# Performance work log

Measured on AMD Instinct MI355X. Metric: run time of the kernel, lower is better.

Reference implementation:

```python
import jax, jax.numpy as jnp
import numpy as np

EPS = 1e-5
D_MODEL, D_INNER, D_STATE, DT_RANK, K = 2048, 4096, 16, 128, 4

def setup_inputs() -> dict:
    key = jax.random.key(0)
    ks = jax.random.split(key, 13)
    B = 128
    s = lambda k, shape, sc=0.02: jax.random.normal(k, shape, jnp.float32) * sc
    return {
        "hidden_states": jax.random.normal(ks[0], (B, 1, D_MODEL), jnp.float32),
        "conv_state": jax.random.normal(ks[1], (B, D_INNER, K - 1), jnp.float32),
        "ssm_state": jax.random.normal(ks[2], (B, D_INNER, D_STATE), jnp.float32),
        "norm_w": jnp.ones((D_MODEL,), jnp.float32),
        "in_proj_w": s(ks[3], (2 * D_INNER, D_MODEL)),           # no bias (HF Mamba default)
        "conv_w": s(ks[4], (D_INNER, K), 0.1),                    # depthwise conv kernel
        "conv_b": s(ks[5], (D_INNER,), 0.1),
        "x_proj_w": s(ks[6], (DT_RANK + 2 * D_STATE, D_INNER)),
        "dt_proj_w": s(ks[7], (D_INNER, DT_RANK)),
        "dt_proj_b": s(ks[8], (D_INNER,), 0.1),
        "A_log": jnp.log(jnp.broadcast_to(jnp.arange(1, D_STATE + 1, dtype=jnp.float32), (D_INNER, D_STATE))),
        "D": jnp.ones((D_INNER,), jnp.float32),
        "out_proj_w": s(ks[9], (D_MODEL, D_INNER)),               # no bias
    }

def reference(hidden_states, conv_state, ssm_state, norm_w, in_proj_w, conv_w, conv_b,
              x_proj_w, dt_proj_w, dt_proj_b, A_log, D, out_proj_w):
    x = hidden_states[:, 0, :]                                   # (B, d_model)
    # RMSNorm (pre-norm)
    normed = x * jax.lax.rsqrt(jnp.mean(x * x, axis=-1, keepdims=True) + EPS) * norm_w
    # in_proj -> gate z and conv branch xc
    xz = normed @ in_proj_w.T                                    # (B, 2*d_inner)
    xc, z = jnp.split(xz, 2, axis=-1)
    # depthwise causal conv, single-step with rolling cache
    conv_in = jnp.concatenate([conv_state, xc[:, :, None]], axis=-1)  # (B, d_inner, K)
    new_conv_state = conv_in[:, :, 1:]
    xact = jax.nn.silu(jnp.sum(conv_in * conv_w[None], axis=-1) + conv_b)  # (B, d_inner)
    # input-dependent SSM params
    proj = xact @ x_proj_w.T                                     # (B, dt_rank + 2*d_state)
    dt_raw = proj[:, :DT_RANK]
    Bmat = proj[:, DT_RANK:DT_RANK + D_STATE]                    # (B, d_state)
    Cmat = proj[:, DT_RANK + D_STATE:]                           # (B, d_state)
    dt = jax.nn.softplus(dt_raw @ dt_proj_w.T + dt_proj_b)       # (B, d_inner)
    A = -jnp.exp(A_log)                                          # (d_inner, d_state)
    dA = jnp.exp(dt[:, :, None] * A[None])                       # (B, d_inner, d_state)
    dB = dt[:, :, None] * Bmat[:, None, :]
    new_ssm_state = ssm_state * dA + dB * xact[:, :, None]
    y = jnp.sum(new_ssm_state * Cmat[:, None, :], axis=-1) + D * xact
    y = y * jax.nn.silu(z)
    out = y @ out_proj_w.T                                       # (B, d_model)
    output = out[:, None, :] + hidden_states                     # residual add
    return output, new_conv_state, new_ssm_state
```

## Files before the change

### kernel.cpp

```cpp
#include <hip/hip_runtime.h>

typedef __attribute__((ext_vector_type(8))) short bf16x8;
typedef __attribute__((ext_vector_type(4))) float f32x4;
typedef __attribute__((ext_vector_type(8))) unsigned short u16x8;
typedef __attribute__((ext_vector_type(2))) unsigned u32x2;

#define DM 2048
#define DI 4096
#define BATCH 128

__device__ __forceinline__ unsigned short f2bf(float f) {
  union { float f; unsigned u; } v; v.f = f;
  unsigned r = v.u + 0x7FFFu + ((v.u >> 16) & 1u);
  return (unsigned short)(r >> 16);
}
__device__ __forceinline__ float bf2f(unsigned short u) {
  union { unsigned u; float f; } v; v.u = (unsigned)u << 16; return v.f;
}
__device__ __forceinline__ unsigned pk2bf(float lo, float hi) {
  unsigned r;
  asm("v_cvt_pk_bf16_f32 %0, %1, %2" : "=v"(r) : "v"(lo), "v"(hi));
  return r;
}
__device__ __forceinline__ float sigm(float x) { return 1.f / (1.f + __expf(-x)); }

constexpr int BK = 64;
constexpr int LDT = BK + 8;

#define LDREGS(AR, ARF, BR, kb_) do {                                                     \
    int kb = (kb_);                                                                       \
    if constexpr (ABF) {                                                                  \
      _Pragma("unroll") for (int i = 0; i < BM / 32; ++i) {                               \
        int idx = tid + i * 256, r = idx >> 3, c = (idx & 7) * 8;                         \
        AR[i] = *(const u16x8*)&((const unsigned short*)Ag)[(long)(m0 + r) * lda + kb + c]; \
      }                                                                                   \
    } else {                                                                              \
      _Pragma("unroll") for (int i = 0; i < BM / 16; ++i) {                               \
        int idx = tid + i * 256, r = idx >> 4, c = (idx & 15) * 4;                        \
        ARF[i] = *(const f32x4*)&((const float*)Ag)[(long)(m0 + r) * lda + kb + c];       \
      }                                                                                   \
    }                                                                                     \
    _Pragma("unroll") for (int i = 0; i < BN / 16; ++i) {                                 \
      int idx = tid + i * 256, r = idx >> 4, c = (idx & 15) * 4;                          \
      BR[i] = *(const f32x4*)&Bg[(long)(n0 + r) * ldb + kb + c];                          \
    }                                                                                     \
  } while (0)

#define STLDS(AR, ARF, BR, buf_) do {                                                     \
    unsigned short* As_ = lds + (buf_) * BUF;                                             \
    unsigned short* Bs_ = As_ + BM * LDT;                                                 \
    if constexpr (ABF) {                                                                  \
      _Pragma("unroll") for (int i = 0; i < BM / 32; ++i) {                               \
        int idx = tid + i * 256, r = idx >> 3, c = (idx & 7) * 8;                         \
        *(u16x8*)&As_[r * LDT + c] = AR[i];                                               \
      }                                                                                   \
    } else {                                                                              \
      _Pragma("unroll") for (int i = 0; i < BM / 16; ++i) {                               \
        int idx = tid + i * 256, r = idx >> 4, c = (idx & 15) * 4;                        \
        u32x2 o; o[0] = pk2bf(ARF[i][0], ARF[i][1]); o[1] = pk2bf(ARF[i][2], ARF[i][3]); \
        *(u32x2*)&As_[r * LDT + c] = o;                                                   \
      }                                                                                   \
    }                                                                                     \
    _Pragma("unroll") for (int i = 0; i < BN / 16; ++i) {                                 \
      int idx = tid + i * 256, r = idx >> 4, c = (idx & 15) * 4;                          \
      u32x2 o; o[0] = pk2bf(BR[i][0], BR[i][1]); o[1] = pk2bf(BR[i][2], BR[i][3]);       \
      *(u32x2*)&Bs_[r * LDT + c] = o;                                                     \
    }                                                                                     \
  } while (0)

#define COMPUTE(buf_) do {                                                                \
    const unsigned short* As_ = lds + (buf_) * BUF;                                       \
    const unsigned short* Bs_ = As_ + BM * LDT;                                           \
    _Pragma("unroll") for (int kk = 0; kk < BK; kk += 32) {                               \
      int kr = kk + lhi * 8;                                                              \
      bf16x8 af[MI], bfr[NF];                                                             \
      _Pragma("unroll") for (int mi = 0; mi < MI; ++mi)                                   \
        af[mi] = *(const bf16x8*)&As_[(wm * (BM / 2) + mi * 16 + llo) * LDT + kr];        \
      _Pragma("unroll") for (int ni = 0; ni < NF; ++ni)                                   \
        bfr[ni] = *(const bf16x8*)&Bs_[(wn * 16 * NF + ni * 16 + llo) * LDT + kr];        \
      _Pragma("unroll") for (int mi = 0; mi < MI; ++mi)                                   \
        _Pragma("unroll") for (int ni = 0; ni < NF; ++ni)                                 \
          acc[mi * NF + ni] = __builtin_amdgcn_mfma_f32_16x16x32_bf16(                    \
              af[mi], bfr[ni], acc[mi * NF + ni], 0, 0, 0);                               \
    }                                                                                     \
  } while (0)

template<int BM, int BN, bool ABF>
__device__ __forceinline__ void gemmMN(const void* Ag, int lda, const float* Bg, int ldb,
                                       int m0, int n0, int k0, int k1, unsigned short* lds,
                                       f32x4* acc) {
  constexpr int NF = BN / 32;
  constexpr int MI = BM / 32;
  constexpr int BUF = (BM + BN) * LDT;
  const int tid = threadIdx.x, lane = tid & 63, wave = tid >> 6;
  const int wm = wave >> 1, wn = wave & 1, llo = lane & 15, lhi = lane >> 4;

  u16x8 ar0[ABF ? BM / 32 : 1], ar1[ABF ? BM / 32 : 1];
  f32x4 arf0[ABF ? 1 : BM / 16], arf1[ABF ? 1 : BM / 16];
  f32x4 br0[BN / 16], br1[BN / 16];

  const int nt = (k1 - k0) / BK;
  LDREGS(ar0, arf0, br0, k0);
  LDREGS(ar1, arf1, br1, k0 + BK);
  STLDS(ar0, arf0, br0, 0);
  __syncthreads();
  int t = 0;
  while (true) {
    if (t + 2 < nt) LDREGS(ar0, arf0, br0, k0 + (t + 2) * BK);
    COMPUTE(0);
    if (t + 1 < nt) STLDS(ar1, arf1, br1, 1);
    __syncthreads();
    if (++t == nt) break;
    if (t + 2 < nt) LDREGS(ar1, arf1, br1, k0 + (t + 2) * BK);
    COMPUTE(1);
    if (t + 1 < nt) STLDS(ar0, arf0, br0, 0);
    __syncthreads();
    if (++t == nt) break;
  }
}

__global__ __launch_bounds__(256) void k1_rmsnorm(const float* __restrict__ hs,
                                                  const float* __restrict__ nw,
                                                  unsigned short* __restrict__ normed) {
  int b = blockIdx.x, tid = threadIdx.x;
  const float* xr = hs + (long)b * DM;
  f32x4 v0 = *(const f32x4*)&xr[tid * 4];
  f32x4 v1 = *(const f32x4*)&xr[(tid + 256) * 4];
  float ss = v0[0]*v0[0] + v0[1]*v0[1] + v0[2]*v0[2] + v0[3]*v0[3]
           + v1[0]*v1[0] + v1[1]*v1[1] + v1[2]*v1[2] + v1[3]*v1[3];
  for (int off = 32; off; off >>= 1) ss += __shfl_xor(ss, off);
  __shared__ float red[4];
  if ((tid & 63) == 0) red[tid >> 6] = ss;
  __syncthreads();
  ss = red[0] + red[1] + red[2] + red[3];
  float rstd = rsqrtf(ss * (1.f / DM) + 1e-5f);
  f32x4 w0 = *(const f32x4*)&nw[tid * 4];
  f32x4 w1 = *(const f32x4*)&nw[(tid + 256) * 4];
  u32x2 o0, o1;
  o0[0] = pk2bf(v0[0] * rstd * w0[0], v0[1] * rstd * w0[1]);
  o0[1] = pk2bf(v0[2] * rstd * w0[2], v0[3] * rstd * w0[3]);
  o1[0] = pk2bf(v1[0] * rstd * w1[0], v1[1] * rstd * w1[1]);
  o1[1] = pk2bf(v1[2] * rstd * w1[2], v1[3] * rstd * w1[3]);
  *(u32x2*)&normed[(long)b * DM + tid * 4] = o0;
  *(u32x2*)&normed[(long)b * DM + (tid + 256) * 4] = o1;
}

__global__ __launch_bounds__(256) void k2_inproj(const unsigned short* __restrict__ normed,
                                                 const float* __restrict__ W,
                                                 float* __restrict__ xzp) {
  __shared__ unsigned short lds[2 * (128 + 64) * LDT];
  f32x4 acc[8] = {};
  int bn = blockIdx.x, sk = blockIdx.y;
  gemmMN<128, 64, true>(normed, DM, W, DM, 0, bn * 64, sk * 512, sk * 512 + 512, lds, acc);
  int tid = threadIdx.x, lane = tid & 63, wave = tid >> 6, wm = wave >> 1, wn = wave & 1;
  int llo = lane & 15, lhi = lane >> 4;
  float* dst = xzp + (long)sk * (BATCH * 8192);
#pragma unroll
  for (int mi = 0; mi < 4; ++mi)
#pragma unroll
    for (int ni = 0; ni < 2; ++ni)
#pragma unroll
      for (int r = 0; r < 4; ++r) {
        int b = wm * 64 + mi * 16 + lhi * 4 + r;
        int n = bn * 64 + wn * 32 + ni * 16 + llo;
        dst[(long)b * 8192 + n] = acc[mi * 2 + ni][r];
      }
}

__global__ __launch_bounds__(256) void e2_conv(const float* __restrict__ xzp,
                                               const float* __restrict__ conv_state,
                                               const float* __restrict__ conv_w,
                                               const float* __restrict__ conv_b,
                                               float* __restrict__ out_ncs,
                                               float* __restrict__ xact_f,
                                               unsigned short* __restrict__ xact_b,
                                               unsigned short* __restrict__ szb) {
  int p = blockIdx.x * 256 + threadIdx.x;
  int b = p >> 12, n = p & 4095;
  long base = (long)b * 8192 + n;
  float xc = 0.f, z = 0.f;
#pragma unroll
  for (int s = 0; s < 4; ++s) {
    xc += xzp[(long)s * (BATCH * 8192) + base];
    z  += xzp[(long)s * (BATCH * 8192) + base + DI];
  }
  const float* cs = conv_state + (long)p * 3;
  float c0 = cs[0], c1 = cs[1], c2 = cs[2];
  f32x4 cw = *(const f32x4*)&conv_w[n * 4];
  float xs = c0 * cw[0] + c1 * cw[1] + c2 * cw[2] + xc * cw[3] + conv_b[n];
  float xa = xs * sigm(xs);
  float* ncs = out_ncs + (long)p * 3;
  ncs[0] = c1; ncs[1] = c2; ncs[2] = xc;
  xact_f[p] = xa;
  xact_b[p] = f2bf(xa);
  szb[p] = f2bf(z * sigm(z));
}

__global__ __launch_bounds__(256) void k3_xproj(const unsigned short* __restrict__ xact_b,
                                                const float* __restrict__ XW,
                                                float* __restrict__ projp) {
  __shared__ unsigned short lds[2 * (128 + 32) * LDT];
  f32x4 acc[4] = {};
  int bn = blockIdx.x, kc = blockIdx.y;
  gemmMN<128, 32, true>(xact_b, DI, XW, DI, 0, bn * 32, kc * 128, kc * 128 + 128, lds, acc);
  int tid = threadIdx.x, lane = tid & 63, wave = tid >> 6, wm = wave >> 1, wn = wave & 1;
  int llo = lane & 15, lhi = lane >> 4;
  int n = bn * 32 + wn * 16 + llo;
  float* dst = projp + (long)kc * (BATCH * 160);
#pragma unroll
  for (int mi = 0; mi < 4; ++mi)
#pragma unroll
    for (int r = 0; r < 4; ++r) {
      int b = wm * 64 + mi * 16 + lhi * 4 + r;
      dst[b * 160 + n] = acc[mi][r];
    }
}

__global__ __launch_bounds__(256) void k3r_reduce(const float* __restrict__ projp,
                                                  float* __restrict__ proj) {
  int t = blockIdx.x * 256 + threadIdx.x;
  f32x4 s = {};
#pragma unroll
  for (int k = 0; k < 32; ++k) {
    f32x4 v = *(const f32x4*)&projp[(long)k * (BATCH * 160) + t * 4];
    s[0] += v[0]; s[1] += v[1]; s[2] += v[2]; s[3] += v[3];
  }
  *(f32x4*)&proj[t * 4] = s;
}

__global__ __launch_bounds__(256) void k45_dtssm(const float* __restrict__ proj,
                                                 const float* __restrict__ DW,
                                                 const float* __restrict__ dtb,
                                                 const float* __restrict__ A_log,
                                                 const float* __restrict__ Dp,
                                                 const float* __restrict__ ssm,
                                                 const float* __restrict__ xact_f,
                                                 const unsigned short* __restrict__ szb,
                                                 float* __restrict__ out_nss,
                                                 unsigned short* __restrict__ yz_b) {
  __shared__ unsigned short lds[2 * (32 + 32) * LDT];
  f32x4 acc[1] = {};
  int nb = blockIdx.x, mb = blockIdx.y;
  gemmMN<32, 32, false>(proj, 160, DW, 128, mb * 32, nb * 32, 0, 128, lds, acc);
  int tid = threadIdx.x, lane = tid & 63, wave = tid >> 6, wm = wave >> 1, wn = wave & 1;
  int llo = lane & 15, lhi = lane >> 4;
  int n = nb * 32 + wn * 16 + llo;
  float dtbn = dtb[n], Dn = Dp[n];
  f32x4 Al0 = *(const f32x4*)&A_log[n * 16];
  f32x4 Al1 = *(const f32x4*)&A_log[n * 16 + 4];
  f32x4 Al2 = *(const f32x4*)&A_log[n * 16 + 8];
  f32x4 Al3 = *(const f32x4*)&A_log[n * 16 + 12];
  float aS[16];
#pragma unroll
  for (int j = 0; j < 4; ++j) {
    aS[j] = -__expf(Al0[j]); aS[4 + j] = -__expf(Al1[j]);
    aS[8 + j] = -__expf(Al2[j]); aS[12 + j] = -__expf(Al3[j]);
  }
#pragma unroll
  for (int r = 0; r < 4; ++r) {
    int b = mb * 32 + wm * 16 + lhi * 4 + r;
    long p = (long)b * DI + n;
    float v = acc[0][r] + dtbn;
    float dtv = (v > 20.f) ? v : log1pf(__expf(v));
    float xa = xact_f[p];
    const float* Bp = proj + b * 160 + 128;
    const float* Cp = proj + b * 160 + 144;
    const float* sp = ssm + p * 16;
    float* np = out_nss + p * 16;
    float y = 0.f;
#pragma unroll
    for (int q = 0; q < 4; ++q) {
      f32x4 sv = *(const f32x4*)&sp[q * 4];
      f32x4 Bv = *(const f32x4*)&Bp[q * 4];
      f32x4 Cv = *(const f32x4*)&Cp[q * 4];
      f32x4 nv;
#pragma unroll
      for (int j = 0; j < 4; ++j) {
        float dA = __expf(dtv * aS[q * 4 + j]);
        nv[j] = sv[j] * dA + dtv * Bv[j] * xa;
        y += nv[j] * Cv[j];
      }
      *(f32x4*)&np[q * 4] = nv;
    }
    yz_b[p] = f2bf((y + Dn * xa) * bf2f(szb[p]));
  }
}

__global__ __launch_bounds__(256) void k5_outproj(const unsigned short* __restrict__ yz_b,
                                                  const float* __restrict__ OW,
                                                  float* __restrict__ op) {
  __shared__ unsigned short lds[2 * (128 + 32) * LDT];
  f32x4 acc[4] = {};
  int bn = blockIdx.x, sk = blockIdx.y;
  gemmMN<128, 32, true>(yz_b, DI, OW, DI, 0, bn * 32, sk * 512, sk * 512 + 512, lds, acc);
  int tid = threadIdx.x, lane = tid & 63, wave = tid >> 6, wm = wave >> 1, wn = wave & 1;
  int llo = lane & 15, lhi = lane >> 4;
  int n = bn * 32 + wn * 16 + llo;
  float* dst = op + (long)sk * (BATCH * DM);
#pragma unroll
  for (int mi = 0; mi < 4; ++mi)
#pragma unroll
    for (int r = 0; r < 4; ++r) {
      int b = wm * 64 + mi * 16 + lhi * 4 + r;
      dst[(long)b * DM + n] = acc[mi][r];
    }
}

__global__ __launch_bounds__(256) void k7_out(const float* __restrict__ op,
                                              const float* __restrict__ hs,
                                              float* __restrict__ outp) {
  int t = blockIdx.x * 256 + threadIdx.x;
  f32x4 s = *(const f32x4*)&hs[t * 4];
#pragma unroll
  for (int k = 0; k < 8; ++k) {
    f32x4 v = *(const f32x4*)&op[(long)k * (BATCH * DM) + t * 4];
    s[0] += v[0]; s[1] += v[1]; s[2] += v[2]; s[3] += v[3];
  }
  *(f32x4*)&outp[t * 4] = s;
}

extern "C" void kernel_launch(void* const* d_in, const int* in_sizes, int n_in, void* d_out,
                              int out_size, void* d_ws, size_t ws_size, hipStream_t stream) {
  const float* hs         = (const float*)d_in[0];
  const float* conv_state = (const float*)d_in[1];
  const float* ssm        = (const float*)d_in[2];
  const float* norm_w     = (const float*)d_in[3];
  const float* in_proj_w  = (const float*)d_in[4];
  const float* conv_w     = (const float*)d_in[5];
  const float* conv_b     = (const float*)d_in[6];
  const float* x_proj_w   = (const float*)d_in[7];
  const float* dt_proj_w  = (const float*)d_in[8];
  const float* dt_proj_b  = (const float*)d_in[9];
  const float* A_log      = (const float*)d_in[10];
  const float* Dp         = (const float*)d_in[11];
  const float* out_proj_w = (const float*)d_in[12];

  float* outp    = (float*)d_out;
  float* out_ncs = outp + 262144;
  float* out_nss = outp + 262144 + 1572864;

  char* ws = (char*)d_ws;
  unsigned short* normed = (unsigned short*)(ws);
  float*          xact_f = (float*)(ws + (1l << 20));
  unsigned short* xact_b = (unsigned short*)(ws + (3l << 20));
  unsigned short* szb    = (unsigned short*)(ws + (4l << 20));
  float*          proj   = (float*)(ws + (5l << 20));
  float*          projp  = (float*)(ws + (6l << 20));
  float*          xzp    = (float*)(ws + (9l << 20));
  float*          op     = (float*)(ws + (25l << 20));
  unsigned short* yz_b   = (unsigned short*)(ws + (34l << 20));

  hipLaunchKernelGGL(k1_rmsnorm, dim3(128), dim3(256), 0, stream, hs, norm_w, normed);
  hipLaunchKernelGGL(k2_inproj, dim3(128, 4), dim3(256), 0, stream, normed, in_proj_w, xzp);
  hipLaunchKernelGGL(e2_conv, dim3(2048), dim3(256), 0, stream, xzp, conv_state, conv_w, conv_b,
                     out_ncs, xact_f, xact_b, szb);
  hipLaunchKernelGGL(k3_xproj, dim3(5, 32), dim3(256), 0, stream, xact_b, x_proj_w, projp);
  hipLaunchKernelGGL(k3r_reduce, dim3(20), dim3(256), 0, stream, projp, proj);
  hipLaunchKernelGGL(k45_dtssm, dim3(128, 4), dim3(256), 0, stream, proj, dt_proj_w, dt_proj_b,
                     A_log, Dp, ssm, xact_f, szb, out_nss, yz_b);
  hipLaunchKernelGGL(k5_outproj, dim3(64, 8), dim3(256), 0, stream, yz_b, out_proj_w, op);
  hipLaunchKernelGGL(k7_out, dim3(256), dim3(256), 0, stream, op, hs, outp);
}
```

Baseline: 77.65 us.

## Load fp32 weights straight into MFMA registers and store in_proj partials as bf16

Adds a skinny GEMM path (gemmS) where each lane loads its fp32 weight fragment from global memory directly into registers and converts it to bf16 for the MFMA. Only the activation tile goes through LDS, which removes the weight LDS staging and halves shared memory per block. In_proj now uses 32-column tiles over twice as many blocks, writes its split-K partials as bf16 instead of fp32, and the GEMM kernels gain a min-blocks occupancy hint. The risk is less coalesced weight loads and some lost precision in the split-K partial sums.

```diff
diff --git a/kernel.cpp b/kernel.cpp
--- a/kernel.cpp
+++ b/kernel.cpp
@@ -4,6 +4,7 @@
 typedef __attribute__((ext_vector_type(4))) float f32x4;
 typedef __attribute__((ext_vector_type(8))) unsigned short u16x8;
 typedef __attribute__((ext_vector_type(2))) unsigned u32x2;
+typedef __attribute__((ext_vector_type(4))) unsigned u32x4u;
 
 #define DM 2048
 #define DI 4096
@@ -27,93 +28,131 @@
 constexpr int BK = 64;
 constexpr int LDT = BK + 8;
 
-#define LDREGS(AR, ARF, BR, kb_) do {                                                     \
-    int kb = (kb_);                                                                       \
-    if constexpr (ABF) {                                                                  \
-      _Pragma("unroll") for (int i = 0; i < BM / 32; ++i) {                               \
-        int idx = tid + i * 256, r = idx >> 3, c = (idx & 7) * 8;                         \
-        AR[i] = *(const u16x8*)&((const unsigned short*)Ag)[(long)(m0 + r) * lda + kb + c]; \
-      }                                                                                   \
-    } else {                                                                              \
-      _Pragma("unroll") for (int i = 0; i < BM / 16; ++i) {                               \
-        int idx = tid + i * 256, r = idx >> 4, c = (idx & 15) * 4;                        \
-        ARF[i] = *(const f32x4*)&((const float*)Ag)[(long)(m0 + r) * lda + kb + c];       \
-      }                                                                                   \
+#define LDA_S(AR, kb_) do { int kb = (kb_);                                   \
+    _Pragma("unroll") for (int i = 0; i < 4; ++i) {                           \
+      int idx = tid + i * 256, r = idx >> 3, c = (idx & 7) * 8;               \
+      AR[i] = *(const u16x8*)&Ab[(long)r * lda + kb + c];                     \
+    } } while (0)
+
+#define STA_S(AR, buf_) do {                                                  \
+    unsigned short* As_ = lds + (buf_) * (128 * LDT);                         \
+    _Pragma("unroll") for (int i = 0; i < 4; ++i) {                           \
+      int idx = tid + i * 256, r = idx >> 3, c = (idx & 7) * 8;               \
+      *(u16x8*)&As_[r * LDT + c] = AR[i];                                     \
+    } } while (0)
+
+#define LDB_S(BB, kb_) do { int kb = (kb_);                                   \
+    const float* bp = &Bg[(long)nrow * ldb + kb + lhi * 8];                   \
+    BB[0] = *(const f32x4*)bp;       BB[1] = *(const f32x4*)(bp + 4);         \
+    BB[2] = *(const f32x4*)(bp + 32); BB[3] = *(const f32x4*)(bp + 36);       \
+  } while (0)
+
+#define CMP_S(buf_, BB) do {                                                  \
+    const unsigned short* As_ = lds + (buf_) * (128 * LDT);                   \
+    _Pragma("unroll") for (int q = 0; q < 2; ++q) {                           \
+      int kr = q * 32 + lhi * 8;                                              \
+      bf16x8 af[4];                                                           \
+      _Pragma("unroll") for (int mi = 0; mi < 4; ++mi)                        \
+        af[mi] = *(const bf16x8*)&As_[(wm * 64 + mi * 16 + llo) * LDT + kr];  \
+      union { u32x4u u; bf16x8 h; } cv;                                       \
+      cv.u[0] = pk2bf(BB[2 * q][0], BB[2 * q][1]);                            \
+      cv.u[1] = pk2bf(BB[2 * q][2], BB[2 * q][3]);                            \
+      cv.u[2] = pk2bf(BB[2 * q + 1][0], BB[2 * q + 1][1]);                    \
+      cv.u[3] = pk2bf(BB[2 * q + 1][2], BB[2 * q + 1][3]);                    \
+      _Pragma("unroll") for (int mi = 0; mi < 4; ++mi)                        \
+        acc[mi] = __builtin_amdgcn_mfma_f32_16x16x32_bf16(af[mi], cv.h, acc[mi], 0, 0, 0); \
+    } } while (0)
+
+__device__ __forceinline__ void gemmS(const unsigned short* __restrict__ Ab, int lda,
+                                      const float* __restrict__ Bg, int ldb,
+                                      int n0, int k0, int k1, unsigned short* lds,
+                                      f32x4* acc) {
+  const int tid = threadIdx.x, lane = tid & 63, wave = tid >> 6;
+  const int wm = wave >> 1, wn = wave & 1, llo = lane & 15, lhi = lane >> 4;
+  const int nrow = n0 + wn * 16 + llo;
+
+  u16x8 ar0[4], ar1[4];
+  f32x4 bB0[4], bB1[4];
+
+  const int nt = (k1 - k0) / BK;
+  LDA_S(ar0, k0);
+  LDA_S(ar1, k0 + BK);
+  LDB_S(bB0, k0);
+  STA_S(ar0, 0);
+  __syncthreads();
+  int t = 0;
+  while (true) {
+    if (t + 1 < nt) LDB_S(bB1, k0 + (t + 1) * BK);
+    if (t + 2 < nt) LDA_S(ar0, k0 + (t + 2) * BK);
+    CMP_S(0, bB0);
+    if (t + 1 < nt) STA_S(ar1, 1);
+    __syncthreads();
+    if (++t == nt) break;
+    if (t + 1 < nt) LDB_S(bB0, k0 + (t + 1) * BK);
+    if (t + 2 < nt) LDA_S(ar1, k0 + (t + 2) * BK);
+    CMP_S(1, bB1);
+    if (t + 1 < nt) STA_S(ar0, 0);
+    __syncthreads();
+    if (++t == nt) break;
+  }
+}
+
+#define LDREGS(ARF, BR, kb_) do { int kb = (kb_);                                         \
+    _Pragma("unroll") for (int i = 0; i < 2; ++i) {                                       \
+      int idx = tid + i * 256, r = idx >> 4, c = (idx & 15) * 4;                          \
+      ARF[i] = *(const f32x4*)&((const float*)Ag)[(long)(m0 + r) * lda + kb + c];         \
     }                                                                                     \
-    _Pragma("unroll") for (int i = 0; i < BN / 16; ++i) {                                 \
+    _Pragma("unroll") for (int i = 0; i < 2; ++i) {                                       \
       int idx = tid + i * 256, r = idx >> 4, c = (idx & 15) * 4;                          \
       BR[i] = *(const f32x4*)&Bg[(long)(n0 + r) * ldb + kb + c];                          \
+    } } while (0)
+
+#define STLDS(ARF, BR, buf_) do {                                                         \
+    unsigned short* As_ = lds + (buf_) * BUF;                                             \
+    unsigned short* Bs_ = As_ + 32 * LDT;                                                 \
+    _Pragma("unroll") for (int i = 0; i < 2; ++i) {                                       \
+      int idx = tid + i * 256, r = idx >> 4, c = (idx & 15) * 4;                          \
+      u32x2 o; o[0] = pk2bf(ARF[i][0], ARF[i][1]); o[1] = pk2bf(ARF[i][2], ARF[i][3]);   \
+      *(u32x2*)&As_[r * LDT + c] = o;                                                     \
     }                                                                                     \
-  } while (0)
-
-#define STLDS(AR, ARF, BR, buf_) do {                                                     \
-    unsigned short* As_ = lds + (buf_) * BUF;                                             \
-    unsigned short* Bs_ = As_ + BM * LDT;                                                 \
-    if constexpr (ABF) {                                                                  \
-      _Pragma("unroll") for (int i = 0; i < BM / 32; ++i) {                               \
-        int idx = tid + i * 256, r = idx >> 3, c = (idx & 7) * 8;                         \
-        *(u16x8*)&As_[r * LDT + c] = AR[i];                                               \
-      }                                                                                   \
-    } else {                                                                              \
-      _Pragma("unroll") for (int i = 0; i < BM / 16; ++i) {                               \
-        int idx = tid + i * 256, r = idx >> 4, c = (idx & 15) * 4;                        \
-        u32x2 o; o[0] = pk2bf(ARF[i][0], ARF[i][1]); o[1] = pk2bf(ARF[i][2], ARF[i][3]); \
-        *(u32x2*)&As_[r * LDT + c] = o;                                                   \
-      }                                                                                   \
-    }                                                                                     \
-    _Pragma("unroll") for (int i = 0; i < BN / 16; ++i) {                                 \
+    _Pragma("unroll") for (int i = 0; i < 2; ++i) {                                       \
       int idx = tid + i * 256, r = idx >> 4, c = (idx & 15) * 4;                          \
       u32x2 o; o[0] = pk2bf(BR[i][0], BR[i][1]); o[1] = pk2bf(BR[i][2], BR[i][3]);       \
       *(u32x2*)&Bs_[r * LDT + c] = o;                                                     \
-    }                                                                                     \
-  } while (0)
+    } } while (0)
 
 #define COMPUTE(buf_) do {                                                                \
     const unsigned short* As_ = lds + (buf_) * BUF;                                       \
-    const unsigned short* Bs_ = As_ + BM * LDT;                                           \
+    const unsigned short* Bs_ = As_ + 32 * LDT;                                           \
     _Pragma("unroll") for (int kk = 0; kk < BK; kk += 32) {                               \
       int kr = kk + lhi * 8;                                                              \
-      bf16x8 af[MI], bfr[NF];                                                             \
-      _Pragma("unroll") for (int mi = 0; mi < MI; ++mi)                                   \
-        af[mi] = *(const bf16x8*)&As_[(wm * (BM / 2) + mi * 16 + llo) * LDT + kr];        \
-      _Pragma("unroll") for (int ni = 0; ni < NF; ++ni)                                   \
-        bfr[ni] = *(const bf16x8*)&Bs_[(wn * 16 * NF + ni * 16 + llo) * LDT + kr];        \
-      _Pragma("unroll") for (int mi = 0; mi < MI; ++mi)                                   \
-        _Pragma("unroll") for (int ni = 0; ni < NF; ++ni)                                 \
-          acc[mi * NF + ni] = __builtin_amdgcn_mfma_f32_16x16x32_bf16(                    \
-              af[mi], bfr[ni], acc[mi * NF + ni], 0, 0, 0);                               \
-    }                                                                                     \
-  } while (0)
-
-template<int BM, int BN, bool ABF>
-__device__ __forceinline__ void gemmMN(const void* Ag, int lda, const float* Bg, int ldb,
+      bf16x8 af = *(const bf16x8*)&As_[(wm * 16 + llo) * LDT + kr];                       \
+      bf16x8 bfr = *(const bf16x8*)&Bs_[(wn * 16 + llo) * LDT + kr];                      \
+      acc[0] = __builtin_amdgcn_mfma_f32_16x16x32_bf16(af, bfr, acc[0], 0, 0, 0);         \
+    } } while (0)
+
+__device__ __forceinline__ void gemm32(const void* Ag, int lda, const float* Bg, int ldb,
                                        int m0, int n0, int k0, int k1, unsigned short* lds,
                                        f32x4* acc) {
-  constexpr int NF = BN / 32;
-  constexpr int MI = BM / 32;
-  constexpr int BUF = (BM + BN) * LDT;
+  constexpr int BUF = 64 * LDT;
   const int tid = threadIdx.x, lane = tid & 63, wave = tid >> 6;
   const int wm = wave >> 1, wn = wave & 1, llo = lane & 15, lhi = lane >> 4;
-
-  u16x8 ar0[ABF ? BM / 32 : 1], ar1[ABF ? BM / 32 : 1];
-  f32x4 arf0[ABF ? 1 : BM / 16], arf1[ABF ? 1 : BM / 16];
-  f32x4 br0[BN / 16], br1[BN / 16];
-
+  f32x4 arf0[2], arf1[2], br0[2], br1[2];
   const int nt = (k1 - k0) / BK;
-  LDREGS(ar0, arf0, br0, k0);
-  LDREGS(ar1, arf1, br1, k0 + BK);
-  STLDS(ar0, arf0, br0, 0);
+  LDREGS(arf0, br0, k0);
+  LDREGS(arf1, br1, k0 + BK);
+  STLDS(arf0, br0, 0);
   __syncthreads();
   int t = 0;
   while (true) {
-    if (t + 2 < nt) LDREGS(ar0, arf0, br0, k0 + (t + 2) * BK);
+    if (t + 2 < nt) LDREGS(arf0, br0, k0 + (t + 2) * BK);
     COMPUTE(0);
-    if (t + 1 < nt) STLDS(ar1, arf1, br1, 1);
+    if (t + 1 < nt) STLDS(arf1, br1, 1);
     __syncthreads();
     if (++t == nt) break;
-    if (t + 2 < nt) LDREGS(ar1, arf1, br1, k0 + (t + 2) * BK);
+    if (t + 2 < nt) LDREGS(arf1, br1, k0 + (t + 2) * BK);
     COMPUTE(1);
-    if (t + 1 < nt) STLDS(ar0, arf0, br0, 0);
+    if (t + 1 < nt) STLDS(arf0, br0, 0);
     __syncthreads();
     if (++t == nt) break;
   }
@@ -145,29 +184,27 @@
   *(u32x2*)&normed[(long)b * DM + (tid + 256) * 4] = o1;
 }
 
-__global__ __launch_bounds__(256) void k2_inproj(const unsigned short* __restrict__ normed,
-                                                 const float* __restrict__ W,
-                                                 float* __restrict__ xzp) {
-  __shared__ unsigned short lds[2 * (128 + 64) * LDT];
-  f32x4 acc[8] = {};
+__global__ __launch_bounds__(256, 4) void k2_inproj(const unsigned short* __restrict__ normed,
+                                                    const float* __restrict__ W,
+                                                    unsigned short* __restrict__ xzp) {
+  __shared__ unsigned short lds[2 * 128 * LDT];
+  f32x4 acc[4] = {};
   int bn = blockIdx.x, sk = blockIdx.y;
-  gemmMN<128, 64, true>(normed, DM, W, DM, 0, bn * 64, sk * 512, sk * 512 + 512, lds, acc);
+  gemmS(normed, DM, W, DM, bn * 32, sk * 512, sk * 512 + 512, lds, acc);
   int tid = threadIdx.x, lane = tid & 63, wave = tid >> 6, wm = wave >> 1, wn = wave & 1;
   int llo = lane & 15, lhi = lane >> 4;
-  float* dst = xzp + (long)sk * (BATCH * 8192);
+  int n = bn * 32 + wn * 16 + llo;
+  unsigned short* dst = xzp + (long)sk * (BATCH * 8192);
 #pragma unroll
   for (int mi = 0; mi < 4; ++mi)
 #pragma unroll
-    for (int ni = 0; ni < 2; ++ni)
-#pragma unroll
-      for (int r = 0; r < 4; ++r) {
-        int b = wm * 64 + mi * 16 + lhi * 4 + r;
-        int n = bn * 64 + wn * 32 + ni * 16 + llo;
-        dst[(long)b * 8192 + n] = acc[mi * 2 + ni][r];
-      }
-}
-
-__global__ __launch_bounds__(256) void e2_conv(const float* __restrict__ xzp,
+    for (int r = 0; r < 4; ++r) {
+      int b = wm * 64 + mi * 16 + lhi * 4 + r;
+      dst[(long)b * 8192 + n] = f2bf(acc[mi][r]);
+    }
+}
+
+__global__ __launch_bounds__(256) void e2_conv(const unsigned short* __restrict__ xzp,
                                                const float* __restrict__ conv_state,
                                                const float* __restrict__ conv_w,
                                                const float* __restrict__ conv_b,
@@ -181,8 +218,8 @@
   float xc = 0.f, z = 0.f;
 #pragma unroll
   for (int s = 0; s < 4; ++s) {
-    xc += xzp[(long)s * (BATCH * 8192) + base];
-    z  += xzp[(long)s * (BATCH * 8192) + base + DI];
+    xc += bf2f(xzp[(long)s * (BATCH * 8192) + base]);
+    z  += bf2f(xzp[(long)s * (BATCH * 8192) + base + DI]);
   }
   const float* cs = conv_state + (long)p * 3;
   float c0 = cs[0], c1 = cs[1], c2 = cs[2];
@@ -196,13 +233,13 @@
   szb[p] = f2bf(z * sigm(z));
 }
 
-__global__ __launch_bounds__(256) void k3_xproj(const unsigned short* __restrict__ xact_b,
-                                                const float* __restrict__ XW,
-                                                float* __restrict__ projp) {
-  __shared__ unsigned short lds[2 * (128 + 32) * LDT];
+__global__ __launch_bounds__(256, 4) void k3_xproj(const unsigned short* __restrict__ xact_b,
+                                                   const float* __restrict__ XW,
+                                                   float* __restrict__ projp) {
+  __shared__ unsigned short lds[2 * 128 * LDT];
   f32x4 acc[4] = {};
   int bn = blockIdx.x, kc = blockIdx.y;
-  gemmMN<128, 32, true>(xact_b, DI, XW, DI, 0, bn * 32, kc * 128, kc * 128 + 128, lds, acc);
+  gemmS(xact_b, DI, XW, DI, bn * 32, kc * 128, kc * 128 + 128, lds, acc);
   int tid = threadIdx.x, lane = tid & 63, wave = tid >> 6, wm = wave >> 1, wn = wave & 1;
   int llo = lane & 15, lhi = lane >> 4;
   int n = bn * 32 + wn * 16 + llo;
@@ -238,10 +275,10 @@
                                                  const unsigned short* __restrict__ szb,
                                                  float* __restrict__ out_nss,
                                                  unsigned short* __restrict__ yz_b) {
-  __shared__ unsigned short lds[2 * (32 + 32) * LDT];
+  __shared__ unsigned short lds[2 * 64 * LDT];
   f32x4 acc[1] = {};
   int nb = blockIdx.x, mb = blockIdx.y;
-  gemmMN<32, 32, false>(proj, 160, DW, 128, mb * 32, nb * 32, 0, 128, lds, acc);
+  gemm32(proj, 160, DW, 128, mb * 32, nb * 32, 0, 128, lds, acc);
   int tid = threadIdx.x, lane = tid & 63, wave = tid >> 6, wm = wave >> 1, wn = wave & 1;
   int llo = lane & 15, lhi = lane >> 4;
   int n = nb * 32 + wn * 16 + llo;
@@ -286,13 +323,13 @@
   }
 }
 
-__global__ __launch_bounds__(256) void k5_outproj(const unsigned short* __restrict__ yz_b,
-                                                  const float* __restrict__ OW,
-                                                  float* __restrict__ op) {
-  __shared__ unsigned short lds[2 * (128 + 32) * LDT];
+__global__ __launch_bounds__(256, 4) void k5_outproj(const unsigned short* __restrict__ yz_b,
+                                                     const float* __restrict__ OW,
+                                                     float* __restrict__ op) {
+  __shared__ unsigned short lds[2 * 128 * LDT];
   f32x4 acc[4] = {};
   int bn = blockIdx.x, sk = blockIdx.y;
-  gemmMN<128, 32, true>(yz_b, DI, OW, DI, 0, bn * 32, sk * 512, sk * 512 + 512, lds, acc);
+  gemmS(yz_b, DI, OW, DI, bn * 32, sk * 512, sk * 512 + 512, lds, acc);
   int tid = threadIdx.x, lane = tid & 63, wave = tid >> 6, wm = wave >> 1, wn = wave & 1;
   int llo = lane & 15, lhi = lane >> 4;
   int n = bn * 32 + wn * 16 + llo;
@@ -346,12 +383,12 @@
   unsigned short* szb    = (unsigned short*)(ws + (4l << 20));
   float*          proj   = (float*)(ws + (5l << 20));
   float*          projp  = (float*)(ws + (6l << 20));
-  float*          xzp    = (float*)(ws + (9l << 20));
-  float*          op     = (float*)(ws + (25l << 20));
-  unsigned short* yz_b   = (unsigned short*)(ws + (34l << 20));
+  unsigned short* xzp    = (unsigned short*)(ws + (9l << 20));
+  float*          op     = (float*)(ws + (18l << 20));
+  unsigned short* yz_b   = (unsigned short*)(ws + (27l << 20));
 
   hipLaunchKernelGGL(k1_rmsnorm, dim3(128), dim3(256), 0, stream, hs, norm_w, normed);
-  hipLaunchKernelGGL(k2_inproj, dim3(128, 4), dim3(256), 0, stream, normed, in_proj_w, xzp);
+  hipLaunchKernelGGL(k2_inproj, dim3(256, 4), dim3(256), 0, stream, normed, in_proj_w, xzp);
   hipLaunchKernelGGL(e2_conv, dim3(2048), dim3(256), 0, stream, xzp, conv_state, conv_w, conv_b,
                      out_ncs, xact_f, xact_b, szb);
   hipLaunchKernelGGL(k3_xproj, dim3(5, 32), dim3(256), 0, stream, xact_b, x_proj_w, projp);
```

New measurement: 84.89 us. 1.09x slower.
